# Kernel optimization log

Measured on AMD Instinct MI355X. Metric: run time of the kernel, lower is better.

The kernel has to match this reference:

```python
import jax, jax.numpy as jnp
import numpy as np

DIM = 192
NUM_HEADS = 4
B, H, W = 2, 256, 256
EPS = 1e-12  # torch F.normalize default eps


def setup_inputs() -> dict:
    key = jax.random.key(0)
    k1, k2, k3 = jax.random.split(key, 3)
    x = jax.random.normal(k1, (B, DIM, H, W), dtype=jnp.float32)
    # depthwise qkv conv: groups=DIM, each group maps 1 in-ch -> 3 out-ch; torch OIHW layout (3*DIM, 1, 3, 3)
    w_qkv = jax.random.normal(k2, (3 * DIM, 1, 3, 3), dtype=jnp.float32) * 0.1
    temperature = jnp.ones((NUM_HEADS, 1, 1), dtype=jnp.float32)
    # 1x1 projection conv, stored as [out, in]
    w_proj = jax.random.normal(k3, (DIM, DIM), dtype=jnp.float32) * (1.0 / np.sqrt(DIM))
    return {"x": x, "w_qkv": w_qkv, "temperature": temperature, "w_proj": w_proj}


def reference(x, w_qkv, temperature, w_proj):
    b, c, h, w = x.shape
    num_heads = temperature.shape[0]
    ch = c // num_heads  # channels per head
    # grouped (depthwise) 3x3 conv producing qkv; torch grouped-conv channel order
    # matches feature_group_count ordering (3 consecutive out-chs per group)... but
    # note torch chunk(3, dim=1) splits the 3*c output into contiguous thirds, so
    # q gets out-channels [0, c), etc. We replicate exactly with same layout.
    qkv = jax.lax.conv_general_dilated(
        x, w_qkv, window_strides=(1, 1), padding=((1, 1), (1, 1)),
        feature_group_count=c,
        dimension_numbers=("NCHW", "OIHW", "NCHW"))
    q, k, v = jnp.split(qkv, 3, axis=1)  # each [b, c, h, w]
    q = q.reshape(b, num_heads, ch, h * w)
    k = k.reshape(b, num_heads, ch, h * w)
    v = v.reshape(b, num_heads, ch, h * w)
    # L2 normalize along spatial dim (torch F.normalize with eps clamp)
    q = q / jnp.maximum(jnp.linalg.norm(q, axis=-1, keepdims=True), EPS)
    k = k / jnp.maximum(jnp.linalg.norm(k, axis=-1, keepdims=True), EPS)
    # channel-channel cosine attention, [b, head, ch, ch] (small)
    attn = jnp.einsum("bhcn,bhdn->bhcd", q, k) * temperature
    attn = jax.nn.softmax(attn, axis=-1)
    out = jnp.einsum("bhcd,bhdn->bhcn", attn, v).reshape(b, c, h, w)
    # 1x1 projection conv
    out = jnp.einsum("oi,bihw->bohw", w_proj, out)
    return out
```

## Files before the change

### kernel.cpp

```cpp
#include <hip/hip_runtime.h>
#include <math.h>

#define BB 2
#define CC 192
#define NH 4
#define CH 48
#define SRCP 16
#define HH 256
#define WW 256
#define NPIX (HH*WW)

typedef __attribute__((ext_vector_type(8))) short short8;
typedef __attribute__((ext_vector_type(4))) float f4;

static __device__ __forceinline__ unsigned short f2bf(float f) {
    union { float f; unsigned int u; } c; c.f = f;
    unsigned int r = c.u + 0x7fffu + ((c.u >> 16) & 1u);
    return (unsigned short)(r >> 16);
}

__global__ __launch_bounds__(256, 2) void k_conv(
    const float* __restrict__ x, const float* __restrict__ wqkv,
    unsigned short* __restrict__ vws, float* __restrict__ Sws,
    float* __restrict__ sqws)
{
    __shared__ float wlds[3*CH*9];
    __shared__ unsigned int qk32[2][CH][132];

    const int tid = threadIdx.x;
    const int hd = blockIdx.x;
    const int y  = blockIdx.y;
    const int b  = blockIdx.z;

    for (int i = tid; i < 3*CH*9; i += 256) {
        int type = i / (CH*9);
        int rem  = i - type*(CH*9);
        wlds[i] = wqkv[type*(CC*9) + hd*(CH*9) + rem];
    }
    __syncthreads();

    {
        const int xp = tid;
        const int y0 = (y > 0) ? (y-1) : 0;
        const int y2 = (y < HH-1) ? (y+1) : y;
        const int xl = (xp > 0) ? (xp-1) : 0;
        const int xr = (xp < WW-1) ? (xp+1) : xp;
        const float my0 = (y > 0) ? 1.f : 0.f;
        const float my2 = (y < HH-1) ? 1.f : 0.f;
        const float mx0 = (xp > 0) ? 1.f : 0.f;
        const float mx2 = (xp < WW-1) ? 1.f : 0.f;
        const float m00 = my0*mx0, m02 = my0*mx2, m20 = my2*mx0, m22 = my2*mx2;

        #pragma unroll
        for (int type = 0; type < 2; ++type) {
            const int srcbase = type*64 + SRCP*hd;
            const float* wt = &wlds[type*(CH*9)];
            for (int g = 0; g < SRCP; ++g) {
                const float* base = x + ((size_t)(b*CC + srcbase + g)*HH)*WW;
                const float* r0 = base + (size_t)y0*WW;
                const float* r1 = base + (size_t)y *WW;
                const float* r2 = base + (size_t)y2*WW;
                float a00 = r0[xl]*m00, a01 = r0[xp]*my0, a02 = r0[xr]*m02;
                float a10 = r1[xl]*mx0, a11 = r1[xp],     a12 = r1[xr]*mx2;
                float a20 = r2[xl]*m20, a21 = r2[xp]*my2, a22 = r2[xr]*m22;
                #pragma unroll
                for (int r = 0; r < 3; ++r) {
                    const int cl = 3*g + r;
                    const float* w = wt + cl*9;
                    float val = a00*w[0] + a01*w[1] + a02*w[2]
                              + a10*w[3] + a11*w[4] + a12*w[5]
                              + a20*w[6] + a21*w[7] + a22*w[8];
                    ((unsigned short*)&qk32[type][cl][0])[xp] = f2bf(val);
                }
            }
        }

        unsigned int vpack[24];
        {
            const int srcbase = 128 + SRCP*hd;
            const float* wt = &wlds[2*(CH*9)];
            #pragma unroll
            for (int g = 0; g < SRCP; ++g) {
                const float* base = x + ((size_t)(b*CC + srcbase + g)*HH)*WW;
                const float* r0 = base + (size_t)y0*WW;
                const float* r1 = base + (size_t)y *WW;
                const float* r2 = base + (size_t)y2*WW;
                float a00 = r0[xl]*m00, a01 = r0[xp]*my0, a02 = r0[xr]*m02;
                float a10 = r1[xl]*mx0, a11 = r1[xp],     a12 = r1[xr]*mx2;
                float a20 = r2[xl]*m20, a21 = r2[xp]*my2, a22 = r2[xr]*m22;
                #pragma unroll
                for (int r = 0; r < 3; ++r) {
                    const int cl = 3*g + r;
                    const float* w = wt + cl*9;
                    float val = a00*w[0] + a01*w[1] + a02*w[2]
                              + a10*w[3] + a11*w[4] + a12*w[5]
                              + a20*w[6] + a21*w[7] + a22*w[8];
                    unsigned int u = f2bf(val);
                    if (cl & 1) vpack[cl >> 1] |= (u << 16);
                    else        vpack[cl >> 1]  = u;
                }
            }
        }
        {
            unsigned short* vp = vws + ((size_t)b*NPIX + (size_t)y*WW + xp)*CC + hd*CH;
            #pragma unroll
            for (int st = 0; st < 6; ++st) {
                uint4 u; u.x = vpack[st*4+0]; u.y = vpack[st*4+1];
                         u.z = vpack[st*4+2]; u.w = vpack[st*4+3];
                *(uint4*)(vp + st*8) = u;
            }
        }
    }
    __syncthreads();

    if (tid < 2*CH) {
        const int which = tid / CH;
        const int cl = tid - which*CH;
        const uint4* row = (const uint4*)&qk32[which][cl][0];
        float ssum = 0.f;
        for (int j = 0; j < 32; ++j) {
            uint4 u = row[j];
            #pragma unroll
            for (int q4 = 0; q4 < 4; ++q4) {
                unsigned int w = (&u.x)[q4];
                float lo = __uint_as_float(w << 16);
                float hi = __uint_as_float(w & 0xffff0000u);
                ssum = fmaf(lo, lo, ssum);
                ssum = fmaf(hi, hi, ssum);
            }
        }
        atomicAdd(&sqws[((b*NH + hd)*2 + which)*CH + cl], ssum);
    }

    {
        const int lane = tid & 63;
        const int wv = tid >> 6;
        const int m = lane & 15, quad = lane >> 4;
        for (int p = wv; p < 9; p += 4) {
            const int ct = p / 3, dt = p - ct*3;
            f4 acc = {0.f, 0.f, 0.f, 0.f};
            const char* qbase = (const char*)&qk32[0][ct*16 + m][0] + quad*16;
            const char* kbase = (const char*)&qk32[1][dt*16 + m][0] + quad*16;
            #pragma unroll
            for (int ks = 0; ks < 8; ++ks) {
                short8 afr = *(const short8*)(qbase + ks*64);
                short8 bfr = *(const short8*)(kbase + ks*64);
                acc = __builtin_amdgcn_mfma_f32_16x16x32_bf16(afr, bfr, acc, 0, 0, 0);
            }
            const int c0 = ct*16 + quad*4, d = dt*16 + m;
            float* Sp = Sws + ((size_t)(b*NH + hd)*CH + c0)*CH + d;
            #pragma unroll
            for (int r = 0; r < 4; ++r) atomicAdd(Sp + r*CH, acc[r]);
        }
    }
}

__global__ __launch_bounds__(256) void k_attn(
    const float* __restrict__ Sws, const float* __restrict__ sqws,
    const float* __restrict__ temp, const float* __restrict__ wproj,
    unsigned short* __restrict__ W2bf)
{
    __shared__ float att[CH][CH+1];
    __shared__ float wp[CC][CH+1];
    __shared__ float nrm[2][CH];

    const int tid = threadIdx.x;
    const int b  = blockIdx.x >> 2;
    const int hd = blockIdx.x & 3;

    if (tid < 2*CH) {
        int which = tid / CH, cl = tid - which*CH;
        nrm[which][cl] = fmaxf(sqrtf(sqws[((b*NH + hd)*2 + which)*CH + cl]), 1e-12f);
    }
    __syncthreads();

    const float tscale = temp[hd];
    for (int m = tid; m < CH*CH; m += 256) {
        int c = m / CH, d = m - c*CH;
        att[c][d] = Sws[((size_t)(b*NH + hd)*CH + c)*CH + d] * tscale
                    / (nrm[0][c] * nrm[1][d]);
    }
    __syncthreads();

    if (tid < CH) {
        float mx = -1e30f;
        for (int d = 0; d < CH; ++d) mx = fmaxf(mx, att[tid][d]);
        float sm = 0.f;
        for (int d = 0; d < CH; ++d) { float e = expf(att[tid][d] - mx); att[tid][d] = e; sm += e; }
        float inv = 1.f / sm;
        for (int d = 0; d < CH; ++d) att[tid][d] *= inv;
    }

    for (int m = tid; m < CC*CH; m += 256) {
        int o = m / CH, il = m - o*CH;
        wp[o][il] = wproj[o*CC + hd*CH + il];
    }
    __syncthreads();

    const int o0  = (tid & 31) * 6;
    const int dl0 = (tid >> 5) * 6;
    float a[6][6];
    #pragma unroll
    for (int i = 0; i < 6; ++i)
        #pragma unroll
        for (int j = 0; j < 6; ++j) a[i][j] = 0.f;
    for (int il = 0; il < CH; ++il) {
        float wv[6], av[6];
        #pragma unroll
        for (int i = 0; i < 6; ++i) wv[i] = wp[o0+i][il];
        #pragma unroll
        for (int j = 0; j < 6; ++j) av[j] = att[il][dl0+j];
        #pragma unroll
        for (int i = 0; i < 6; ++i)
            #pragma unroll
            for (int j = 0; j < 6; ++j)
                a[i][j] = fmaf(wv[i], av[j], a[i][j]);
    }
    #pragma unroll
    for (int i = 0; i < 6; ++i)
        #pragma unroll
        for (int j = 0; j < 6; ++j)
            W2bf[((size_t)b*CC + o0 + i)*CC + hd*CH + dl0 + j] = f2bf(a[i][j]);
}

__global__ __launch_bounds__(256, 2) void k_out(
    const unsigned short* __restrict__ vws, const unsigned short* __restrict__ W2bf,
    float* __restrict__ out)
{
    __shared__ unsigned short w2l[CC][200];

    const int tid = threadIdx.x;
    const int b  = blockIdx.y;
    const int n0 = blockIdx.x * 128;

    {
        const uint4* src = (const uint4*)(W2bf + (size_t)b*CC*CC);
        for (int i = tid; i < CC*24; i += 256) {
            int o = i / 24, c = i - o*24;
            *(uint4*)&w2l[o][c*8] = src[i];
        }
    }
    __syncthreads();

    const int lane = tid & 63;
    const int wv = tid >> 6;
    const int m0  = (wv & 1) * 96;
    const int nn0 = (wv >> 1) * 64;
    const int m = lane & 15, quad = lane >> 4;

    f4 acc[6][4];
    #pragma unroll
    for (int mt = 0; mt < 6; ++mt)
        #pragma unroll
        for (int nt = 0; nt < 4; ++nt) acc[mt][nt] = (f4){0.f, 0.f, 0.f, 0.f};

    const unsigned short* vb = vws + ((size_t)b*NPIX + n0 + nn0 + m)*CC + quad*8;

    #pragma unroll
    for (int ks = 0; ks < 6; ++ks) {
        short8 bfr[4];
        #pragma unroll
        for (int nt = 0; nt < 4; ++nt)
            bfr[nt] = *(const short8*)(vb + (size_t)(nt*16)*CC + ks*32);
        short8 afr[6];
        #pragma unroll
        for (int mt = 0; mt < 6; ++mt)
            afr[mt] = *(const short8*)&w2l[m0 + mt*16 + m][ks*32 + quad*8];
        #pragma unroll
        for (int mt = 0; mt < 6; ++mt)
            #pragma unroll
            for (int nt = 0; nt < 4; ++nt)
                acc[mt][nt] = __builtin_amdgcn_mfma_f32_16x16x32_bf16(afr[mt], bfr[nt], acc[mt][nt], 0, 0, 0);
    }

    #pragma unroll
    for (int mt = 0; mt < 6; ++mt) {
        const int o = m0 + mt*16 + quad*4;
        #pragma unroll
        for (int nt = 0; nt < 4; ++nt) {
            const int px = n0 + nn0 + nt*16 + m;
            float* op = out + ((size_t)(b*CC + o))*NPIX + px;
            #pragma unroll
            for (int r = 0; r < 4; ++r) op[(size_t)r*NPIX] = acc[mt][nt][r];
        }
    }
}

extern "C" void kernel_launch(void* const* d_in, const int* in_sizes, int n_in,
                              void* d_out, int out_size, void* d_ws, size_t ws_size,
                              hipStream_t stream)
{
    const float* x     = (const float*)d_in[0];
    const float* wqkv  = (const float*)d_in[1];
    const float* temp  = (const float*)d_in[2];
    const float* wproj = (const float*)d_in[3];
    float* out = (float*)d_out;
    (void)in_sizes; (void)n_in; (void)out_size; (void)ws_size;

    unsigned short* vws = (unsigned short*)d_ws;
    const size_t VBYTES = (size_t)BB*CC*NPIX*sizeof(unsigned short);
    float* Sws  = (float*)((char*)d_ws + VBYTES);
    float* sqws = Sws + (size_t)BB*NH*CH*CH;
    unsigned short* W2bf = (unsigned short*)(sqws + (size_t)BB*NH*2*CH);

    hipMemsetAsync(Sws, 0, (size_t)(BB*NH*CH*CH + BB*NH*2*CH)*sizeof(float), stream);
    k_conv<<<dim3(NH, HH, BB), 256, 0, stream>>>(x, wqkv, vws, Sws, sqws);
    k_attn<<<dim3(BB*NH), 256, 0, stream>>>(Sws, sqws, temp, wproj, W2bf);
    k_out<<<dim3(NPIX/128, BB), 256, 0, stream>>>(vws, W2bf, out);
}
```

Measured before the change: 322.9 us.

## Restructure depthwise conv so each wave handles one source channel with float4 rows

The qkv conv is rewritten so that each wave processes one source channel across the full image row. Each lane loads float4 row chunks and takes its horizontal neighbours via lane shuffles, replacing nine scalar loads per pixel. The next channel's rows are prefetched while the current one is computed, and weights are read from global memory as wave-uniform values instead of being staged in LDS. Squared norms are now reduced with wave shuffles, bf16 packing uses the hardware v_cvt_pk_bf16_f32 instruction, and V is staged in LDS and then transposed to its pixel-major global layout. The trade-off is more LDS for the V tile and added shuffle overhead.

Result: slower. 480.0 us (+48.7%).

```diff
diff --git a/kernel.cpp b/kernel.cpp
--- a/kernel.cpp
+++ b/kernel.cpp
@@ -5,7 +5,6 @@
 #define CC 192
 #define NH 4
 #define CH 48
-#define SRCP 16
 #define HH 256
 #define WW 256
 #define NPIX (HH*WW)
@@ -17,6 +16,12 @@
     union { float f; unsigned int u; } c; c.f = f;
     unsigned int r = c.u + 0x7fffu + ((c.u >> 16) & 1u);
     return (unsigned short)(r >> 16);
+}
+
+static __device__ __forceinline__ unsigned int cvtpk_bf16(float lo, float hi) {
+    unsigned int r;
+    asm("v_cvt_pk_bf16_f32 %0, %1, %2" : "=v"(r) : "v"(lo), "v"(hi));
+    return r;
 }
 
 __global__ __launch_bounds__(256, 2) void k_conv(
@@ -24,131 +29,136 @@
     unsigned short* __restrict__ vws, float* __restrict__ Sws,
     float* __restrict__ sqws)
 {
-    __shared__ float wlds[3*CH*9];
-    __shared__ unsigned int qk32[2][CH][132];
-
-    const int tid = threadIdx.x;
+    __shared__ unsigned int qkv[3][CH][132];
+
+    const int tid  = threadIdx.x;
+    const int lane = tid & 63;
+    const int wv   = tid >> 6;
     const int hd = blockIdx.x;
     const int y  = blockIdx.y;
     const int b  = blockIdx.z;
 
-    for (int i = tid; i < 3*CH*9; i += 256) {
-        int type = i / (CH*9);
-        int rem  = i - type*(CH*9);
-        wlds[i] = wqkv[type*(CC*9) + hd*(CH*9) + rem];
-    }
-    __syncthreads();
-
+    const int y0 = (y > 0) ? (y-1) : 0;
+    const int y2 = (y < HH-1) ? (y+1) : y;
+    const float my0 = (y > 0) ? 1.f : 0.f;
+    const float my2 = (y < HH-1) ? 1.f : 0.f;
+
+    int t = __builtin_amdgcn_readfirstlane(wv);
+    float4 c0, c1, c2;
     {
-        const int xp = tid;
-        const int y0 = (y > 0) ? (y-1) : 0;
-        const int y2 = (y < HH-1) ? (y+1) : y;
-        const int xl = (xp > 0) ? (xp-1) : 0;
-        const int xr = (xp < WW-1) ? (xp+1) : xp;
-        const float my0 = (y > 0) ? 1.f : 0.f;
-        const float my2 = (y < HH-1) ? 1.f : 0.f;
-        const float mx0 = (xp > 0) ? 1.f : 0.f;
-        const float mx2 = (xp < WW-1) ? 1.f : 0.f;
-        const float m00 = my0*mx0, m02 = my0*mx2, m20 = my2*mx0, m22 = my2*mx2;
-
-        #pragma unroll
-        for (int type = 0; type < 2; ++type) {
-            const int srcbase = type*64 + SRCP*hd;
-            const float* wt = &wlds[type*(CH*9)];
-            for (int g = 0; g < SRCP; ++g) {
-                const float* base = x + ((size_t)(b*CC + srcbase + g)*HH)*WW;
-                const float* r0 = base + (size_t)y0*WW;
-                const float* r1 = base + (size_t)y *WW;
-                const float* r2 = base + (size_t)y2*WW;
-                float a00 = r0[xl]*m00, a01 = r0[xp]*my0, a02 = r0[xr]*m02;
-                float a10 = r1[xl]*mx0, a11 = r1[xp],     a12 = r1[xr]*mx2;
-                float a20 = r2[xl]*m20, a21 = r2[xp]*my2, a22 = r2[xr]*m22;
-                #pragma unroll
-                for (int r = 0; r < 3; ++r) {
-                    const int cl = 3*g + r;
-                    const float* w = wt + cl*9;
-                    float val = a00*w[0] + a01*w[1] + a02*w[2]
-                              + a10*w[3] + a11*w[4] + a12*w[5]
-                              + a20*w[6] + a21*w[7] + a22*w[8];
-                    ((unsigned short*)&qk32[type][cl][0])[xp] = f2bf(val);
-                }
-            }
-        }
-
-        unsigned int vpack[24];
+        const int type = t >> 4, g = t & 15;
+        const float* base = x + ((size_t)(b*CC + type*64 + hd*16 + g))*NPIX;
+        c0 = *(const float4*)(base + (size_t)y0*WW + 4*lane);
+        c1 = *(const float4*)(base + (size_t)y *WW + 4*lane);
+        c2 = *(const float4*)(base + (size_t)y2*WW + 4*lane);
+        c0.x *= my0; c0.y *= my0; c0.z *= my0; c0.w *= my0;
+        c2.x *= my2; c2.y *= my2; c2.z *= my2; c2.w *= my2;
+    }
+    for (int i = 0; i < 12; ++i) {
+        const int ii = (i < 11) ? (i + 1) : 11;
+        const int tn = __builtin_amdgcn_readfirstlane(wv + 4*ii);
+        float4 n0, n1, n2;
         {
-            const int srcbase = 128 + SRCP*hd;
-            const float* wt = &wlds[2*(CH*9)];
-            #pragma unroll
-            for (int g = 0; g < SRCP; ++g) {
-                const float* base = x + ((size_t)(b*CC + srcbase + g)*HH)*WW;
-                const float* r0 = base + (size_t)y0*WW;
-                const float* r1 = base + (size_t)y *WW;
-                const float* r2 = base + (size_t)y2*WW;
-                float a00 = r0[xl]*m00, a01 = r0[xp]*my0, a02 = r0[xr]*m02;
-                float a10 = r1[xl]*mx0, a11 = r1[xp],     a12 = r1[xr]*mx2;
-                float a20 = r2[xl]*m20, a21 = r2[xp]*my2, a22 = r2[xr]*m22;
-                #pragma unroll
-                for (int r = 0; r < 3; ++r) {
-                    const int cl = 3*g + r;
-                    const float* w = wt + cl*9;
-                    float val = a00*w[0] + a01*w[1] + a02*w[2]
-                              + a10*w[3] + a11*w[4] + a12*w[5]
-                              + a20*w[6] + a21*w[7] + a22*w[8];
-                    unsigned int u = f2bf(val);
-                    if (cl & 1) vpack[cl >> 1] |= (u << 16);
-                    else        vpack[cl >> 1]  = u;
-                }
-            }
-        }
+            const int type = tn >> 4, g = tn & 15;
+            const float* base = x + ((size_t)(b*CC + type*64 + hd*16 + g))*NPIX;
+            n0 = *(const float4*)(base + (size_t)y0*WW + 4*lane);
+            n1 = *(const float4*)(base + (size_t)y *WW + 4*lane);
+            n2 = *(const float4*)(base + (size_t)y2*WW + 4*lane);
+            n0.x *= my0; n0.y *= my0; n0.z *= my0; n0.w *= my0;
+            n2.x *= my2; n2.y *= my2; n2.z *= my2; n2.w *= my2;
+        }
+
+        const int type = t >> 4, g = t & 15;
+        const float* wp = wqkv + type*(CC*9) + hd*(CH*9) + g*27;
+        float w[27];
+        #pragma unroll
+        for (int j = 0; j < 27; ++j) w[j] = wp[j];
+
+        float a0[4] = {0.f,0.f,0.f,0.f};
+        float a1[4] = {0.f,0.f,0.f,0.f};
+        float a2[4] = {0.f,0.f,0.f,0.f};
+        #pragma unroll
+        for (int j = 0; j < 3; ++j) {
+            const float4 rr = (j == 0) ? c0 : ((j == 1) ? c1 : c2);
+            float lft = __shfl_up(rr.w, 1);   lft = (lane == 0)  ? 0.f : lft;
+            float rgt = __shfl_down(rr.x, 1); rgt = (lane == 63) ? 0.f : rgt;
+            const float t0[4] = {lft,  rr.x, rr.y, rr.z};
+            const float t1[4] = {rr.x, rr.y, rr.z, rr.w};
+            const float t2[4] = {rr.y, rr.z, rr.w, rgt };
+            #pragma unroll
+            for (int p = 0; p < 4; ++p) {
+                a0[p] = fmaf(w[   3*j], t0[p], fmaf(w[   3*j+1], t1[p], fmaf(w[   3*j+2], t2[p], a0[p])));
+                a1[p] = fmaf(w[ 9+3*j], t0[p], fmaf(w[ 9+3*j+1], t1[p], fmaf(w[ 9+3*j+2], t2[p], a1[p])));
+                a2[p] = fmaf(w[18+3*j], t0[p], fmaf(w[18+3*j+1], t1[p], fmaf(w[18+3*j+2], t2[p], a2[p])));
+            }
+        }
+
+        if (type < 2) {
+            float s0 = 0.f, s1 = 0.f, s2 = 0.f;
+            #pragma unroll
+            for (int p = 0; p < 4; ++p) {
+                s0 = fmaf(a0[p], a0[p], s0);
+                s1 = fmaf(a1[p], a1[p], s1);
+                s2 = fmaf(a2[p], a2[p], s2);
+            }
+            #pragma unroll
+            for (int off = 32; off; off >>= 1) {
+                s0 += __shfl_xor(s0, off);
+                s1 += __shfl_xor(s1, off);
+                s2 += __shfl_xor(s2, off);
+            }
+            if (lane == 0) {
+                float* sq = sqws + ((b*NH + hd)*2 + type)*CH + 3*g;
+                atomicAdd(sq + 0, s0); atomicAdd(sq + 1, s1); atomicAdd(sq + 2, s2);
+            }
+        }
+
         {
-            unsigned short* vp = vws + ((size_t)b*NPIX + (size_t)y*WW + xp)*CC + hd*CH;
-            #pragma unroll
-            for (int st = 0; st < 6; ++st) {
-                uint4 u; u.x = vpack[st*4+0]; u.y = vpack[st*4+1];
-                         u.z = vpack[st*4+2]; u.w = vpack[st*4+3];
-                *(uint4*)(vp + st*8) = u;
-            }
-        }
-    }
-    __syncthreads();
-
-    if (tid < 2*CH) {
-        const int which = tid / CH;
-        const int cl = tid - which*CH;
-        const uint4* row = (const uint4*)&qk32[which][cl][0];
-        float ssum = 0.f;
-        for (int j = 0; j < 32; ++j) {
-            uint4 u = row[j];
-            #pragma unroll
-            for (int q4 = 0; q4 < 4; ++q4) {
-                unsigned int w = (&u.x)[q4];
-                float lo = __uint_as_float(w << 16);
-                float hi = __uint_as_float(w & 0xffff0000u);
-                ssum = fmaf(lo, lo, ssum);
-                ssum = fmaf(hi, hi, ssum);
-            }
-        }
-        atomicAdd(&sqws[((b*NH + hd)*2 + which)*CH + cl], ssum);
-    }
+            uint2 d;
+            d.x = cvtpk_bf16(a0[0], a0[1]); d.y = cvtpk_bf16(a0[2], a0[3]);
+            ((uint2*)&qkv[type][3*g + 0][0])[lane] = d;
+            d.x = cvtpk_bf16(a1[0], a1[1]); d.y = cvtpk_bf16(a1[2], a1[3]);
+            ((uint2*)&qkv[type][3*g + 1][0])[lane] = d;
+            d.x = cvtpk_bf16(a2[0], a2[1]); d.y = cvtpk_bf16(a2[2], a2[3]);
+            ((uint2*)&qkv[type][3*g + 2][0])[lane] = d;
+        }
+
+        t = tn; c0 = n0; c1 = n1; c2 = n2;
+    }
+    __syncthreads();
 
     {
-        const int lane = tid & 63;
-        const int wv = tid >> 6;
+        const unsigned short* vrow = (const unsigned short*)&qkv[2][0][0];
+        unsigned short* vp = vws + ((size_t)b*NPIX + (size_t)y*WW + tid)*CC + hd*CH;
+        unsigned int d[24];
+        #pragma unroll
+        for (int c2 = 0; c2 < 24; ++c2) {
+            unsigned int lo = vrow[(2*c2    )*264 + tid];
+            unsigned int hi = vrow[(2*c2 + 1)*264 + tid];
+            d[c2] = lo | (hi << 16);
+        }
+        #pragma unroll
+        for (int st = 0; st < 6; ++st) {
+            uint4 u; u.x = d[4*st+0]; u.y = d[4*st+1]; u.z = d[4*st+2]; u.w = d[4*st+3];
+            *(uint4*)(vp + st*8) = u;
+        }
+    }
+
+    {
         const int m = lane & 15, quad = lane >> 4;
         for (int p = wv; p < 9; p += 4) {
             const int ct = p / 3, dt = p - ct*3;
             f4 acc = {0.f, 0.f, 0.f, 0.f};
-            const char* qbase = (const char*)&qk32[0][ct*16 + m][0] + quad*16;
-            const char* kbase = (const char*)&qk32[1][dt*16 + m][0] + quad*16;
+            const char* qbase = (const char*)&qkv[0][ct*16 + m][0] + quad*16;
+            const char* kbase = (const char*)&qkv[1][dt*16 + m][0] + quad*16;
             #pragma unroll
             for (int ks = 0; ks < 8; ++ks) {
                 short8 afr = *(const short8*)(qbase + ks*64);
                 short8 bfr = *(const short8*)(kbase + ks*64);
                 acc = __builtin_amdgcn_mfma_f32_16x16x32_bf16(afr, bfr, acc, 0, 0, 0);
             }
-            const int c0 = ct*16 + quad*4, d = dt*16 + m;
-            float* Sp = Sws + ((size_t)(b*NH + hd)*CH + c0)*CH + d;
+            const int c0i = ct*16 + quad*4, dd = dt*16 + m;
+            float* Sp = Sws + ((size_t)(b*NH + hd)*CH + c0i)*CH + dd;
             #pragma unroll
             for (int r = 0; r < 4; ++r) atomicAdd(Sp + r*CH, acc[r]);
         }
```
